# Kernel tuning notes

Hardware: AMD Instinct MI355X
Metric: run time of the kernel (lower is better)

## Reference

```python
import jax, jax.numpy as jnp
import numpy as np

B, S, D, A = 32, 2048, 512, 256


def setup_inputs() -> dict:
    key = jax.random.key(0)
    ks = jax.random.split(key, 9)
    enc = jax.random.normal(ks[0], (B, S, D), dtype=jnp.float32)
    dec = jax.random.normal(ks[1], (B, 1, D), dtype=jnp.float32)
    prev = jax.random.uniform(ks[2], (B, S), dtype=jnp.float32)
    prev = prev / jnp.sum(prev, axis=1, keepdims=True)  # normalized prev attention
    noise = jax.random.normal(ks[3], (B, S), dtype=jnp.float32)
    W = jax.random.normal(ks[4], (A, D), dtype=jnp.float32) / np.sqrt(D)
    V = jax.random.normal(ks[5], (A, D), dtype=jnp.float32) / np.sqrt(D)
    b = jax.random.normal(ks[6], (A,), dtype=jnp.float32)
    v_w = jax.random.normal(ks[7], (1, A), dtype=jnp.float32)
    v_g = jnp.full((1,), np.sqrt(1.0 / A), dtype=jnp.float32)  # weight_norm g init
    v_bias = jax.random.normal(ks[8], (1,), dtype=jnp.float32)
    r = jnp.full((1,), -4.0, dtype=jnp.float32)
    return {"encoder_outputs": enc, "decoder_h": dec, "prev_alpha": prev,
            "noise": noise, "W": W, "V": V, "b": b, "v_w": v_w,
            "v_g": v_g, "v_bias": v_bias, "r": r}


def reference(encoder_outputs, decoder_h, prev_alpha, noise, W, V, b, v_w, v_g, v_bias, r):
    # Energy: tanh-MLP Bahdanau score with weight-normed output projection
    h = jnp.tanh(jnp.einsum('bsd,ad->bsa', encoder_outputs, W)
                 + jnp.einsum('bod,ad->boa', decoder_h, V)  # [B,1,A] broadcasts over S
                 + b)
    w_eff = v_g * v_w / jnp.linalg.norm(v_w)       # weight_norm: g * v / ||v||
    energy = jnp.einsum('bsa,oa->bso', h, w_eff)[..., 0] + v_bias[0] + r[0]  # [B,S]
    # Soft monotonic attention recurrence
    p_select = jax.nn.sigmoid(energy + noise)
    log1mp = jnp.log(jnp.clip(1.0 - p_select, 1e-10, 1.0))
    cumprod_1mp = jnp.exp(jnp.cumsum(log1mp, axis=1))  # safe_cumprod
    alpha = p_select * cumprod_1mp * jnp.cumsum(prev_alpha / cumprod_1mp, axis=1)
    # Context: enc^T @ alpha
    context = jnp.einsum('bsd,bs->bd', encoder_outputs, alpha)
    return context, alpha
```

## Files before the change

kernel.cpp:

```cpp
#include <hip/hip_runtime.h>
#include <math.h>

#define B_  32
#define S_  2048
#define D_  512
#define A_  256
#define BS_ (B_ * S_)

#define WEFF_OFF  0
#define DEC_OFF   256
#define EPART_OFF 8448
#define CTX_OFF   (8448 + BS_)

typedef _Float16 f16x8 __attribute__((ext_vector_type(8)));
typedef _Float16 half4 __attribute__((ext_vector_type(4)));
typedef float floatx4 __attribute__((ext_vector_type(4)));

__global__ void ma_prep_kernel(const float* __restrict__ v_w,
                               const float* __restrict__ v_g,
                               const float* __restrict__ dec,
                               const float* __restrict__ V,
                               const float* __restrict__ bvec,
                               const float* __restrict__ W,
                               _Float16* __restrict__ W16,
                               float* __restrict__ ws) {
    __shared__ float sh[D_];
    const int bid = blockIdx.x, t = threadIdx.x;
    if (bid == 0) {
        float v = v_w[t];
        float sq = v * v;
        #pragma unroll
        for (int off = 32; off > 0; off >>= 1) sq += __shfl_down(sq, off, 64);
        if ((t & 63) == 0) sh[t >> 6] = sq;
        __syncthreads();
        float n2 = sh[0] + sh[1] + sh[2] + sh[3];
        ws[WEFF_OFF + t] = v_g[0] * v / sqrtf(n2);
    } else if (bid <= B_) {
        const int b = bid - 1;
        sh[t]       = dec[b * D_ + t];
        sh[t + 256] = dec[b * D_ + 256 + t];
        __syncthreads();
        const float4* Vr = (const float4*)(V + (size_t)t * D_);
        float acc = 0.f;
        #pragma unroll 4
        for (int k = 0; k < D_ / 4; ++k) {
            float4 v4 = Vr[k];
            acc = fmaf(v4.x, sh[4*k+0], acc);
            acc = fmaf(v4.y, sh[4*k+1], acc);
            acc = fmaf(v4.z, sh[4*k+2], acc);
            acc = fmaf(v4.w, sh[4*k+3], acc);
        }
        ws[DEC_OFF + b * A_ + t] = acc + bvec[t];
    } else {
        int i = (bid - (B_ + 1)) * 256 + t;
        float4 v = ((const float4*)W)[i];
        half4 h;
        h[0] = (_Float16)v.x; h[1] = (_Float16)v.y;
        h[2] = (_Float16)v.z; h[3] = (_Float16)v.w;
        ((half4*)W16)[i] = h;
    }
}

#define LDST 40
__global__ void ma_energy_mfma(
        const float* __restrict__ enc,
        const _Float16* __restrict__ W16,
        const float* __restrict__ ws_in,
        float* __restrict__ energy) {
    __shared__ __align__(16) _Float16 As[2][64 * LDST];
    __shared__ float red[4][64];

    const int t  = threadIdx.x;
    const int bx = blockIdx.x;
    const size_t R0 = (size_t)bx * 64;
    const int batch = bx >> 5;

    const int lr = t >> 2;
    const int kc = (t & 3) * 8;
    const float* Ag = enc + (R0 + (size_t)lr) * D_ + kc;

    const int lane = t & 63, wn = t >> 6;
    const int fr = lane & 15, kq = lane >> 4;
    const _Float16* Bg = W16 + (size_t)(wn * 64 + fr) * D_ + kq * 8;

    floatx4 acc[4][4];
    #pragma unroll
    for (int m = 0; m < 4; ++m)
        #pragma unroll
        for (int n = 0; n < 4; ++n) acc[m][n] = (floatx4)0.f;

    float4 pa0 = *(const float4*)(Ag);
    float4 pa1 = *(const float4*)(Ag + 4);
    {
        f16x8 h;
        h[0] = (_Float16)pa0.x; h[1] = (_Float16)pa0.y;
        h[2] = (_Float16)pa0.z; h[3] = (_Float16)pa0.w;
        h[4] = (_Float16)pa1.x; h[5] = (_Float16)pa1.y;
        h[6] = (_Float16)pa1.z; h[7] = (_Float16)pa1.w;
        *(f16x8*)&As[0][lr * LDST + kc] = h;
    }
    pa0 = *(const float4*)(Ag + 32);
    pa1 = *(const float4*)(Ag + 36);
    __syncthreads();

    for (int kt = 0; kt < 16; ++kt) {
        const int cur = kt & 1;
        f16x8 bf[4];
        #pragma unroll
        for (int n = 0; n < 4; ++n)
            bf[n] = *(const f16x8*)(Bg + (size_t)(n * 16) * D_ + kt * 32);
        if (kt < 15) {
            f16x8 h;
            h[0] = (_Float16)pa0.x; h[1] = (_Float16)pa0.y;
            h[2] = (_Float16)pa0.z; h[3] = (_Float16)pa0.w;
            h[4] = (_Float16)pa1.x; h[5] = (_Float16)pa1.y;
            h[6] = (_Float16)pa1.z; h[7] = (_Float16)pa1.w;
            *(f16x8*)&As[cur ^ 1][lr * LDST + kc] = h;
        }
        if (kt < 14) {
            pa0 = *(const float4*)(Ag + (kt + 2) * 32);
            pa1 = *(const float4*)(Ag + (kt + 2) * 32 + 4);
        }
        f16x8 af[4];
        #pragma unroll
        for (int m = 0; m < 4; ++m)
            af[m] = *(const f16x8*)&As[cur][(m * 16 + fr) * LDST + kq * 8];
        #pragma unroll
        for (int m = 0; m < 4; ++m)
            #pragma unroll
            for (int n = 0; n < 4; ++n)
                acc[m][n] = __builtin_amdgcn_mfma_f32_16x16x32_f16(af[m], bf[n], acc[m][n], 0, 0, 0);
        __syncthreads();
    }

    const float* weff  = ws_in + WEFF_OFF;
    const float* dterm = ws_in + DEC_OFF + batch * A_;
    float wj[4], dj[4];
    #pragma unroll
    for (int n = 0; n < 4; ++n) {
        int a = wn * 64 + n * 16 + fr;
        wj[n] = weff[a];
        dj[n] = dterm[a];
    }
    #pragma unroll
    for (int m = 0; m < 4; ++m) {
        #pragma unroll
        for (int r = 0; r < 4; ++r) {
            float v = 0.f;
            #pragma unroll
            for (int n = 0; n < 4; ++n) {
                float x = acc[m][n][r] + dj[n];
                float e = __expf(2.f * x);
                v += (1.f - 2.f / (e + 1.f)) * wj[n];
            }
            #pragma unroll
            for (int mask = 1; mask < 16; mask <<= 1)
                v += __shfl_xor(v, mask, 64);
            if (fr == 0)
                red[wn][m * 16 + (kq << 2) + r] = v;
        }
    }
    __syncthreads();
    if (t < 64)
        energy[R0 + t] = red[0][t] + red[1][t] + red[2][t] + red[3][t];
}

__global__ void ma_scan_kernel(const float* __restrict__ energy,
                               const float* __restrict__ noise,
                               const float* __restrict__ prev,
                               const float* __restrict__ v_bias,
                               const float* __restrict__ r,
                               float* __restrict__ alpha_out) {
    int b = blockIdx.x, t = threadIdx.x;
    const float bias = v_bias[0] + r[0];
    int base = b * S_ + t * 8;
    float p[8], av[8], bv[8];
    #pragma unroll
    for (int i = 0; i < 8; ++i) {
        float e = energy[base + i] + bias + noise[base + i];
        float pi = 1.f / (1.f + expf(-e));
        p[i]  = pi;
        av[i] = fmaxf(1.f - pi, 1e-10f);
        bv[i] = prev[base + i];
    }
    float Ai = 1.f, Bi = 0.f;
    #pragma unroll
    for (int i = 0; i < 8; ++i) { Bi = av[i] * Bi + bv[i]; Ai *= av[i]; }
    int lane = t & 63;
    #pragma unroll
    for (int off = 1; off < 64; off <<= 1) {
        float Ap = __shfl_up(Ai, off, 64);
        float Bp = __shfl_up(Bi, off, 64);
        if (lane >= off) { Bi = Ai * Bp + Bi; Ai = Ai * Ap; }
    }
    __shared__ float wA[4], wB[4];
    int w = t >> 6;
    if (lane == 63) { wA[w] = Ai; wB[w] = Bi; }
    __syncthreads();
    float Ax = __shfl_up(Ai, 1, 64);
    float Bx = __shfl_up(Bi, 1, 64);
    if (lane == 0) { Ax = 1.f; Bx = 0.f; }
    float PwA = 1.f, PwB = 0.f;
    for (int q = 0; q < w; ++q) { PwB = wA[q] * PwB + wB[q]; PwA *= wA[q]; }
    float T = Ax * PwB + Bx;
    #pragma unroll
    for (int i = 0; i < 8; ++i) {
        T = av[i] * T + bv[i];
        alpha_out[base + i] = p[i] * T;
    }
}

__global__ void ma_ctxpart_kernel(const float* __restrict__ enc,
                                  const float* __restrict__ alpha,
                                  float* __restrict__ cpart) {
    int b = blockIdx.x, sc = blockIdx.y, t = threadIdx.x;
    const float* e0 = enc + ((size_t)b * S_ + sc * 128) * D_;
    const float* al = alpha + b * S_ + sc * 128;
    float a0 = 0.f, a1 = 0.f;
    for (int s = 0; s < 128; ++s) {
        float avv = al[s];
        a0 = fmaf(e0[(size_t)s * D_ + t], avv, a0);
        a1 = fmaf(e0[(size_t)s * D_ + 256 + t], avv, a1);
    }
    cpart[((size_t)(sc * B_ + b)) * D_ + t]       = a0;
    cpart[((size_t)(sc * B_ + b)) * D_ + 256 + t] = a1;
}

__global__ void ma_ctxreduce_kernel(const float* __restrict__ cpart,
                                    float* __restrict__ ctx) {
    int b = blockIdx.x, t = threadIdx.x;
    #pragma unroll
    for (int h = 0; h < 2; ++h) {
        int d = t + h * 256;
        float s = 0.f;
        #pragma unroll
        for (int q = 0; q < 16; ++q) s += cpart[((size_t)(q * B_ + b)) * D_ + d];
        ctx[b * D_ + d] = s;
    }
}

extern "C" void kernel_launch(void* const* d_in, const int* in_sizes, int n_in,
                              void* d_out, int out_size, void* d_ws, size_t ws_size,
                              hipStream_t stream) {
    const float* enc    = (const float*)d_in[0];
    const float* dec    = (const float*)d_in[1];
    const float* prev   = (const float*)d_in[2];
    const float* noise  = (const float*)d_in[3];
    const float* W      = (const float*)d_in[4];
    const float* V      = (const float*)d_in[5];
    const float* bvec   = (const float*)d_in[6];
    const float* v_w    = (const float*)d_in[7];
    const float* v_g    = (const float*)d_in[8];
    const float* v_bias = (const float*)d_in[9];
    const float* r      = (const float*)d_in[10];

    float* out = (float*)d_out;
    float* ws  = (float*)d_ws;
    float* alpha = out + B_ * D_;
    _Float16* W16 = (_Float16*)(ws + CTX_OFF);

    ma_prep_kernel<<<1 + B_ + 128, 256, 0, stream>>>(v_w, v_g, dec, V, bvec, W, W16, ws);
    ma_energy_mfma<<<1024, 256, 0, stream>>>(enc, W16, ws, ws + EPART_OFF);
    ma_scan_kernel<<<B_, 256, 0, stream>>>(ws + EPART_OFF, noise, prev, v_bias, r, alpha);
    dim3 gc(B_, 16);
    ma_ctxpart_kernel<<<gc, 256, 0, stream>>>(enc, alpha, ws + CTX_OFF);
    ma_ctxreduce_kernel<<<B_, 256, 0, stream>>>(ws + CTX_OFF, out);
}
```

Before: 95.42 us.

## Enlarge energy GEMM tile to 128 rows and stage W in LDS via async loads

The energy MFMA kernel now processes 128 encoder rows per block with 8 waves in a 2x4 layout, so each block covers all 256 A columns. W16 is no longer read by every wave straight from global memory. It is double-buffered into shared memory with global_load_lds and shared across the two row-waves. This halves redundant W traffic per row and uses direct-to-LDS async copies, at the cost of more LDS per block and fewer, larger blocks. No wait or fence is added beyond the existing __syncthreads, which may be enough given how the compiler handles these loads.

```diff
diff --git a/kernel.cpp b/kernel.cpp
--- a/kernel.cpp
+++ b/kernel.cpp
@@ -15,6 +15,12 @@
 typedef _Float16 f16x8 __attribute__((ext_vector_type(8)));
 typedef _Float16 half4 __attribute__((ext_vector_type(4)));
 typedef float floatx4 __attribute__((ext_vector_type(4)));
+
+__device__ __forceinline__ void glds16(const void* g, void* l) {
+    __builtin_amdgcn_global_load_lds(
+        (const __attribute__((address_space(1))) void*)g,
+        (__attribute__((address_space(3))) void*)l, 16, 0, 0);
+}
 
 __global__ void ma_prep_kernel(const float* __restrict__ v_w,
                                const float* __restrict__ v_g,
@@ -61,27 +67,33 @@
     }
 }
 
-#define LDST 40
-__global__ void ma_energy_mfma(
+#define LDSTA 40
+__global__ __launch_bounds__(512) void ma_energy_mfma(
         const float* __restrict__ enc,
         const _Float16* __restrict__ W16,
         const float* __restrict__ ws_in,
         float* __restrict__ energy) {
-    __shared__ __align__(16) _Float16 As[2][64 * LDST];
-    __shared__ float red[4][64];
+    __shared__ __align__(16) _Float16 As[2][128 * LDSTA];
+    __shared__ __align__(16) _Float16 Bs[2][256 * 32];
+    __shared__ float red[4][128];
 
     const int t  = threadIdx.x;
     const int bx = blockIdx.x;
-    const size_t R0 = (size_t)bx * 64;
-    const int batch = bx >> 5;
+    const size_t R0 = (size_t)bx * 128;
+    const int batch = bx >> 4;
 
     const int lr = t >> 2;
     const int kc = (t & 3) * 8;
     const float* Ag = enc + (R0 + (size_t)lr) * D_ + kc;
 
-    const int lane = t & 63, wn = t >> 6;
+    const int lane = t & 63, wid = t >> 6;
+    const int wm = wid >> 2, wn = wid & 3;
     const int fr = lane & 15, kq = lane >> 4;
-    const _Float16* Bg = W16 + (size_t)(wn * 64 + fr) * D_ + kq * 8;
+
+    const _Float16* Bg0 = W16 + (size_t)(wid * 32 + (lane >> 2)) * D_ + (lane & 3) * 8;
+    const _Float16* Bg1 = Bg0 + (size_t)16 * D_;
+    const int bdst0 = (wid * 32) * 32;
+    const int bdst1 = (wid * 32 + 16) * 32;
 
     floatx4 acc[4][4];
     #pragma unroll
@@ -89,42 +101,47 @@
         #pragma unroll
         for (int n = 0; n < 4; ++n) acc[m][n] = (floatx4)0.f;
 
-    float4 pa0 = *(const float4*)(Ag);
-    float4 pa1 = *(const float4*)(Ag + 4);
+    glds16(Bg0, &Bs[0][bdst0]);
+    glds16(Bg1, &Bs[0][bdst1]);
+    float4 a0 = *(const float4*)(Ag);
+    float4 a1 = *(const float4*)(Ag + 4);
     {
         f16x8 h;
-        h[0] = (_Float16)pa0.x; h[1] = (_Float16)pa0.y;
-        h[2] = (_Float16)pa0.z; h[3] = (_Float16)pa0.w;
-        h[4] = (_Float16)pa1.x; h[5] = (_Float16)pa1.y;
-        h[6] = (_Float16)pa1.z; h[7] = (_Float16)pa1.w;
-        *(f16x8*)&As[0][lr * LDST + kc] = h;
-    }
-    pa0 = *(const float4*)(Ag + 32);
-    pa1 = *(const float4*)(Ag + 36);
+        h[0] = (_Float16)a0.x; h[1] = (_Float16)a0.y;
+        h[2] = (_Float16)a0.z; h[3] = (_Float16)a0.w;
+        h[4] = (_Float16)a1.x; h[5] = (_Float16)a1.y;
+        h[6] = (_Float16)a1.z; h[7] = (_Float16)a1.w;
+        *(f16x8*)&As[0][lr * LDSTA + kc] = h;
+    }
+    a0 = *(const float4*)(Ag + 32);
+    a1 = *(const float4*)(Ag + 36);
     __syncthreads();
 
     for (int kt = 0; kt < 16; ++kt) {
         const int cur = kt & 1;
-        f16x8 bf[4];
+        if (kt < 15) {
+            glds16(Bg0 + (kt + 1) * 32, &Bs[cur ^ 1][bdst0]);
+            glds16(Bg1 + (kt + 1) * 32, &Bs[cur ^ 1][bdst1]);
+        }
+        f16x8 af[4], bf[4];
+        #pragma unroll
+        for (int m = 0; m < 4; ++m)
+            af[m] = *(const f16x8*)&As[cur][(wm * 64 + m * 16 + fr) * LDSTA + kq * 8];
         #pragma unroll
         for (int n = 0; n < 4; ++n)
-            bf[n] = *(const f16x8*)(Bg + (size_t)(n * 16) * D_ + kt * 32);
+            bf[n] = *(const f16x8*)&Bs[cur][(wn * 64 + n * 16 + fr) * 32 + kq * 8];
         if (kt < 15) {
             f16x8 h;
-            h[0] = (_Float16)pa0.x; h[1] = (_Float16)pa0.y;
-            h[2] = (_Float16)pa0.z; h[3] = (_Float16)pa0.w;
-            h[4] = (_Float16)pa1.x; h[5] = (_Float16)pa1.y;
-            h[6] = (_Float16)pa1.z; h[7] = (_Float16)pa1.w;
-            *(f16x8*)&As[cur ^ 1][lr * LDST + kc] = h;
+            h[0] = (_Float16)a0.x; h[1] = (_Float16)a0.y;
+            h[2] = (_Float16)a0.z; h[3] = (_Float16)a0.w;
+            h[4] = (_Float16)a1.x; h[5] = (_Float16)a1.y;
+            h[6] = (_Float16)a1.z; h[7] = (_Float16)a1.w;
+            *(f16x8*)&As[cur ^ 1][lr * LDSTA + kc] = h;
         }
         if (kt < 14) {
-            pa0 = *(const float4*)(Ag + (kt + 2) * 32);
-            pa1 = *(const float4*)(Ag + (kt + 2) * 32 + 4);
-        }
-        f16x8 af[4];
-        #pragma unroll
-        for (int m = 0; m < 4; ++m)
-            af[m] = *(const f16x8*)&As[cur][(m * 16 + fr) * LDST + kq * 8];
+            a0 = *(const float4*)(Ag + (kt + 2) * 32);
+            a1 = *(const float4*)(Ag + (kt + 2) * 32 + 4);
+        }
         #pragma unroll
         for (int m = 0; m < 4; ++m)
             #pragma unroll
@@ -157,11 +174,11 @@
             for (int mask = 1; mask < 16; mask <<= 1)
                 v += __shfl_xor(v, mask, 64);
             if (fr == 0)
-                red[wn][m * 16 + (kq << 2) + r] = v;
+                red[wn][wm * 64 + m * 16 + (kq << 2) + r] = v;
         }
     }
     __syncthreads();
-    if (t < 64)
+    if (t < 128)
         energy[R0 + t] = red[0][t] + red[1][t] + red[2][t] + red[3][t];
 }
 
@@ -260,7 +277,7 @@
     _Float16* W16 = (_Float16*)(ws + CTX_OFF);
 
     ma_prep_kernel<<<1 + B_ + 128, 256, 0, stream>>>(v_w, v_g, dec, V, bvec, W, W16, ws);
-    ma_energy_mfma<<<1024, 256, 0, stream>>>(enc, W16, ws, ws + EPART_OFF);
+    ma_energy_mfma<<<512, 512, 0, stream>>>(enc, W16, ws, ws + EPART_OFF);
     ma_scan_kernel<<<B_, 256, 0, stream>>>(ws + EPART_OFF, noise, prev, v_bias, r, alpha);
     dim3 gc(B_, 16);
     ma_ctxpart_kernel<<<gc, 256, 0, stream>>>(enc, alpha, ws + CTX_OFF);
```

Result: faster. 85.94 us (-9.9%).

## Load energy GEMM operands directly into registers and split context reduction finer

Applied to the files above, without the earlier changes.

The energy MFMA kernel drops the shared-memory staging of encoder rows and its barriers. Each wave now loads its fp32 A fragments straight from global memory, converts them to fp16 in registers, and double-buffers both A and B in registers across k-steps. The cost is that all four waves in a block fetch the same A rows, so global load traffic grows unless L1/L2 absorbs it. Separately, the context partial-sum kernel splits the sequence into 32 chunks instead of 16, giving more blocks for bandwidth, and the reduce kernel sums 32 partials.

```diff
diff --git a/kernel.cpp b/kernel.cpp
--- a/kernel.cpp
+++ b/kernel.cpp
@@ -61,13 +61,11 @@
     }
 }
 
-#define LDST 40
 __global__ void ma_energy_mfma(
         const float* __restrict__ enc,
         const _Float16* __restrict__ W16,
         const float* __restrict__ ws_in,
         float* __restrict__ energy) {
-    __shared__ __align__(16) _Float16 As[2][64 * LDST];
     __shared__ float red[4][64];
 
     const int t  = threadIdx.x;
@@ -75,12 +73,10 @@
     const size_t R0 = (size_t)bx * 64;
     const int batch = bx >> 5;
 
-    const int lr = t >> 2;
-    const int kc = (t & 3) * 8;
-    const float* Ag = enc + (R0 + (size_t)lr) * D_ + kc;
-
     const int lane = t & 63, wn = t >> 6;
     const int fr = lane & 15, kq = lane >> 4;
+
+    const float*    Ag = enc + (R0 + (size_t)fr) * D_ + kq * 8;
     const _Float16* Bg = W16 + (size_t)(wn * 64 + fr) * D_ + kq * 8;
 
     floatx4 acc[4][4];
@@ -89,48 +85,69 @@
         #pragma unroll
         for (int n = 0; n < 4; ++n) acc[m][n] = (floatx4)0.f;
 
-    float4 pa0 = *(const float4*)(Ag);
-    float4 pa1 = *(const float4*)(Ag + 4);
-    {
-        f16x8 h;
-        h[0] = (_Float16)pa0.x; h[1] = (_Float16)pa0.y;
-        h[2] = (_Float16)pa0.z; h[3] = (_Float16)pa0.w;
-        h[4] = (_Float16)pa1.x; h[5] = (_Float16)pa1.y;
-        h[6] = (_Float16)pa1.z; h[7] = (_Float16)pa1.w;
-        *(f16x8*)&As[0][lr * LDST + kc] = h;
-    }
-    pa0 = *(const float4*)(Ag + 32);
-    pa1 = *(const float4*)(Ag + 36);
-    __syncthreads();
-
-    for (int kt = 0; kt < 16; ++kt) {
-        const int cur = kt & 1;
-        f16x8 bf[4];
-        #pragma unroll
-        for (int n = 0; n < 4; ++n)
-            bf[n] = *(const f16x8*)(Bg + (size_t)(n * 16) * D_ + kt * 32);
-        if (kt < 15) {
-            f16x8 h;
-            h[0] = (_Float16)pa0.x; h[1] = (_Float16)pa0.y;
-            h[2] = (_Float16)pa0.z; h[3] = (_Float16)pa0.w;
-            h[4] = (_Float16)pa1.x; h[5] = (_Float16)pa1.y;
-            h[6] = (_Float16)pa1.z; h[7] = (_Float16)pa1.w;
-            *(f16x8*)&As[cur ^ 1][lr * LDST + kc] = h;
-        }
-        if (kt < 14) {
-            pa0 = *(const float4*)(Ag + (kt + 2) * 32);
-            pa1 = *(const float4*)(Ag + (kt + 2) * 32 + 4);
-        }
-        f16x8 af[4];
-        #pragma unroll
-        for (int m = 0; m < 4; ++m)
-            af[m] = *(const f16x8*)&As[cur][(m * 16 + fr) * LDST + kq * 8];
-        #pragma unroll
-        for (int m = 0; m < 4; ++m)
+    float4 rA[4][2];
+    f16x8  rB0[4], rB1[4];
+
+    #pragma unroll
+    for (int m = 0; m < 4; ++m) {
+        rA[m][0] = *(const float4*)(Ag + m * 16 * D_);
+        rA[m][1] = *(const float4*)(Ag + m * 16 * D_ + 4);
+    }
+    #pragma unroll
+    for (int n = 0; n < 4; ++n)
+        rB0[n] = *(const f16x8*)(Bg + n * 16 * D_);
+
+    #pragma unroll 1
+    for (int kt2 = 0; kt2 < 8; ++kt2) {
+        {
+            f16x8 af[4];
+            #pragma unroll
+            for (int m = 0; m < 4; ++m) {
+                af[m][0] = (_Float16)rA[m][0].x; af[m][1] = (_Float16)rA[m][0].y;
+                af[m][2] = (_Float16)rA[m][0].z; af[m][3] = (_Float16)rA[m][0].w;
+                af[m][4] = (_Float16)rA[m][1].x; af[m][5] = (_Float16)rA[m][1].y;
+                af[m][6] = (_Float16)rA[m][1].z; af[m][7] = (_Float16)rA[m][1].w;
+            }
+            const int ko = (2 * kt2 + 1) * 32;
             #pragma unroll
             for (int n = 0; n < 4; ++n)
-                acc[m][n] = __builtin_amdgcn_mfma_f32_16x16x32_f16(af[m], bf[n], acc[m][n], 0, 0, 0);
-        __syncthreads();
+                rB1[n] = *(const f16x8*)(Bg + n * 16 * D_ + ko);
+            #pragma unroll
+            for (int m = 0; m < 4; ++m) {
+                rA[m][0] = *(const float4*)(Ag + m * 16 * D_ + ko);
+                rA[m][1] = *(const float4*)(Ag + m * 16 * D_ + ko + 4);
+            }
+            #pragma unroll
+            for (int m = 0; m < 4; ++m)
+                #pragma unroll
+                for (int n = 0; n < 4; ++n)
+                    acc[m][n] = __builtin_amdgcn_mfma_f32_16x16x32_f16(af[m], rB0[n], acc[m][n], 0, 0, 0);
+        }
+        {
+            f16x8 af[4];
+            #pragma unroll
+            for (int m = 0; m < 4; ++m) {
+                af[m][0] = (_Float16)rA[m][0].x; af[m][1] = (_Float16)rA[m][0].y;
+                af[m][2] = (_Float16)rA[m][0].z; af[m][3] = (_Float16)rA[m][0].w;
+                af[m][4] = (_Float16)rA[m][1].x; af[m][5] = (_Float16)rA[m][1].y;
+                af[m][6] = (_Float16)rA[m][1].z; af[m][7] = (_Float16)rA[m][1].w;
+            }
+            const int kn = 2 * kt2 + 2;
+            const int ko = (kn < 16 ? kn : 15) * 32;
+            #pragma unroll
+            for (int n = 0; n < 4; ++n)
+                rB0[n] = *(const f16x8*)(Bg + n * 16 * D_ + ko);
+            #pragma unroll
+            for (int m = 0; m < 4; ++m) {
+                rA[m][0] = *(const float4*)(Ag + m * 16 * D_ + ko);
+                rA[m][1] = *(const float4*)(Ag + m * 16 * D_ + ko + 4);
+            }
+            #pragma unroll
+            for (int m = 0; m < 4; ++m)
+                #pragma unroll
+                for (int n = 0; n < 4; ++n)
+                    acc[m][n] = __builtin_amdgcn_mfma_f32_16x16x32_f16(af[m], rB1[n], acc[m][n], 0, 0, 0);
+        }
     }
 
     const float* weff  = ws_in + WEFF_OFF;
@@ -214,10 +231,10 @@
                                   const float* __restrict__ alpha,
                                   float* __restrict__ cpart) {
     int b = blockIdx.x, sc = blockIdx.y, t = threadIdx.x;
-    const float* e0 = enc + ((size_t)b * S_ + sc * 128) * D_;
-    const float* al = alpha + b * S_ + sc * 128;
+    const float* e0 = enc + ((size_t)b * S_ + sc * 64) * D_;
+    const float* al = alpha + b * S_ + sc * 64;
     float a0 = 0.f, a1 = 0.f;
-    for (int s = 0; s < 128; ++s) {
+    for (int s = 0; s < 64; ++s) {
         float avv = al[s];
         a0 = fmaf(e0[(size_t)s * D_ + t], avv, a0);
         a1 = fmaf(e0[(size_t)s * D_ + 256 + t], avv, a1);
@@ -234,7 +251,7 @@
         int d = t + h * 256;
         float s = 0.f;
         #pragma unroll
-        for (int q = 0; q < 16; ++q) s += cpart[((size_t)(q * B_ + b)) * D_ + d];
+        for (int q = 0; q < 32; ++q) s += cpart[((size_t)(q * B_ + b)) * D_ + d];
         ctx[b * D_ + d] = s;
     }
 }
@@ -262,7 +279,7 @@
     ma_prep_kernel<<<1 + B_ + 128, 256, 0, stream>>>(v_w, v_g, dec, V, bvec, W, W16, ws);
     ma_energy_mfma<<<1024, 256, 0, stream>>>(enc, W16, ws, ws + EPART_OFF);
     ma_scan_kernel<<<B_, 256, 0, stream>>>(ws + EPART_OFF, noise, prev, v_bias, r, alpha);
-    dim3 gc(B_, 16);
+    dim3 gc(B_, 32);
     ma_ctxpart_kernel<<<gc, 256, 0, stream>>>(enc, alpha, ws + CTX_OFF);
     ma_ctxreduce_kernel<<<B_, 256, 0, stream>>>(ws + CTX_OFF, out);
 }
```

After: 142.2 us. 49.0% more time.
